# Kernel optimization log

Measured on AMD Instinct MI355X. Metric: run time of the kernel, lower is better.

## Reference

```python
import jax, jax.numpy as jnp
import numpy as np

NODE_DIM = 256
OUTPUT_DIM = 256
NUM_HOPS = 4
NUM_NODES = 25000
NUM_EDGES = 400000
NUM_TYPES = 10
FEAT_DIM = 32


def setup_inputs() -> dict:
    key = jax.random.key(0)
    ks = jax.random.split(key, 12)
    nodes = jax.random.normal(ks[0], (NUM_NODES, FEAT_DIM), dtype=jnp.float32)
    edges = jax.random.randint(ks[1], (2, NUM_EDGES), 0, NUM_NODES, dtype=jnp.int64)
    node_types = jax.random.randint(ks[2], (NUM_NODES,), 0, NUM_TYPES, dtype=jnp.int64)
    s = 0.02
    type_emb = jax.random.normal(ks[3], (NUM_TYPES, NODE_DIM), dtype=jnp.float32) * s
    W_proj = jax.random.normal(ks[4], (FEAT_DIM, NODE_DIM), dtype=jnp.float32) * s
    b_proj = jnp.zeros((NODE_DIM,), dtype=jnp.float32)
    W_msg = jax.random.normal(ks[5], (NUM_HOPS, 2 * NODE_DIM, NODE_DIM), dtype=jnp.float32) * s
    b_msg = jnp.zeros((NUM_HOPS, NODE_DIM), dtype=jnp.float32)
    W_upd = jax.random.normal(ks[6], (NUM_HOPS, 2 * NODE_DIM, NODE_DIM), dtype=jnp.float32) * s
    b_upd = jnp.zeros((NUM_HOPS, NODE_DIM), dtype=jnp.float32)
    W_out = jax.random.normal(ks[7], (NODE_DIM, OUTPUT_DIM), dtype=jnp.float32) * s
    b_out = jnp.zeros((OUTPUT_DIM,), dtype=jnp.float32)
    return {"nodes": nodes, "edges": edges, "node_types": node_types,
            "type_emb": type_emb, "W_proj": W_proj, "b_proj": b_proj,
            "W_msg": W_msg, "b_msg": b_msg, "W_upd": W_upd, "b_upd": b_upd,
            "W_out": W_out, "b_out": b_out}


def reference(nodes, edges, node_types, type_emb, W_proj, b_proj,
              W_msg, b_msg, W_upd, b_upd, W_out, b_out):
    n = nodes.shape[0]
    src, dst = edges[0], edges[1]
    # initial node states: linear proj + type embedding
    h = nodes @ W_proj + b_proj + type_emb[node_types]  # [N, D]
    for i in range(NUM_HOPS):
        edge_feat = jnp.concatenate([h[src], h[dst]], axis=1)      # [E, 2D]
        messages = edge_feat @ W_msg[i] + b_msg[i]                 # [E, D]
        agg = jax.ops.segment_sum(messages, dst, num_segments=n)   # [N, D]
        h = jax.nn.relu(jnp.concatenate([h, agg], axis=1) @ W_upd[i] + b_upd[i])
    graph_embedding = jnp.max(h, axis=0)                           # [D]
    return graph_embedding @ W_out + b_out                          # [output_dim]
```

## Files before the change

### kernel.cpp

```cpp
#include <hip/hip_runtime.h>
#include <hip/hip_bf16.h>

#define NDIM 256
#define FDIM 32
#define HOPS 4
#define NPB 8

typedef __attribute__((ext_vector_type(8))) short short8;
typedef __attribute__((ext_vector_type(4))) float f32x4;
typedef __attribute__((ext_vector_type(2))) float f32x2;

__device__ inline float b2f(unsigned short u) {
    union { unsigned int i; float f; } v; v.i = ((unsigned int)u) << 16; return v.f;
}
__device__ inline unsigned short f2b(float f) {
    union { float f; unsigned int i; } v; v.f = f;
    unsigned int r = v.i + 0x7FFF + ((v.i >> 16) & 1);
    return (unsigned short)(r >> 16);
}
__device__ inline unsigned char f2fp8(float v) {
    return (unsigned char)(__builtin_amdgcn_cvt_pk_fp8_f32(v, v, 0, false) & 0xFF);
}

__global__ __launch_bounds__(256) void prep_mega_kernel(
        const int* __restrict__ dst, int* __restrict__ deg, int E, int histB,
        const float* __restrict__ Wm, const float* __restrict__ Wu,
        const float* __restrict__ bm,
        unsigned short* __restrict__ WtB,
        unsigned short* __restrict__ Am, unsigned short* __restrict__ BmT,
        float* __restrict__ cvec, int* __restrict__ geInt,
        unsigned char* __restrict__ h8row,
        const float* __restrict__ nodes, const int* __restrict__ node_types,
        const float* __restrict__ type_emb, const float* __restrict__ W_proj,
        const float* __restrict__ b_proj,
        unsigned short* __restrict__ h, unsigned char* __restrict__ h8, int n) {
    __shared__ float T[32][33];
    __shared__ float sb[256];
    int b = blockIdx.x;
    int t = threadIdx.x;

    if (b < histB) {
        int e = (b * 256 + t) * 4;
        if (e + 3 < E) {
            int4 d = *(const int4*)(dst + e);
            atomicAdd(&deg[d.x], 1);
            atomicAdd(&deg[d.y], 1);
            atomicAdd(&deg[d.z], 1);
            atomicAdd(&deg[d.w], 1);
        } else {
            for (int k = e; k < E; ++k) atomicAdd(&deg[dst[k]], 1);
        }
    } else if (b < histB + 773) {
        int bb = b - histB;
        if (bb < 256) {
            int hop = bb >> 6;
            int rem = bb & 63;
            int k0 = (rem & 7) * 32, n0 = (rem >> 3) * 32;
            const float* src = Wu + (size_t)hop * 512 * 256;
            unsigned short* dstp = WtB + (size_t)hop * 256 * 256;
            int tr = t >> 5, tc = t & 31;
#pragma unroll
            for (int r = 0; r < 4; ++r) {
                int k = tr + r * 8;
                T[tc][k] = src[(size_t)(k0 + k) * 256 + n0 + tc];
            }
            __syncthreads();
#pragma unroll
            for (int r = 0; r < 4; ++r) {
                int nn = tr + r * 8;
                dstp[(size_t)(n0 + nn) * 256 + k0 + tc] = f2b(T[nn][tc]);
            }
        } else if (bb < 260) {
            int hop = bb - 256;
            sb[t] = bm[hop * 256 + t];
            __syncthreads();
            const float* B = Wu + (size_t)hop * 512 * 256 + (size_t)256 * 256;
            float acc = 0.f;
#pragma unroll 8
            for (int j = 0; j < 256; ++j) acc += sb[j] * B[(size_t)j * 256 + t];
            cvec[hop * 256 + t] = acc;
        } else if (bb == 260) {
            geInt[t] = 0;
            h8row[t] = 0;
        } else if (bb < 517) {
            size_t base = (size_t)(bb - 261) * 2048 + (size_t)t * 8;
            float4 a0 = *(const float4*)(Wm + base);
            float4 a1 = *(const float4*)(Wm + base + 4);
            ushort4 o0, o1;
            o0.x = f2b(a0.x); o0.y = f2b(a0.y); o0.z = f2b(a0.z); o0.w = f2b(a0.w);
            o1.x = f2b(a1.x); o1.y = f2b(a1.y); o1.z = f2b(a1.z); o1.w = f2b(a1.w);
            *(ushort4*)(Am + base) = o0;
            *(ushort4*)(Am + base + 4) = o1;
        } else {
            int tb = bb - 517;
            int hop = tb >> 6;
            int rem = tb & 63;
            int j0 = (rem & 7) * 32, n0 = (rem >> 3) * 32;
            const float* srcp = Wu + (size_t)hop * 512 * 256 + (size_t)256 * 256;
            unsigned short* dstp = BmT + (size_t)hop * 256 * 256;
            int tr = t >> 5, tc = t & 31;
#pragma unroll
            for (int r = 0; r < 4; ++r) {
                int j = tr + r * 8;
                T[tc][j] = srcp[(size_t)(j0 + j) * 256 + n0 + tc];
            }
            __syncthreads();
#pragma unroll
            for (int r = 0; r < 4; ++r) {
                int nn = tr + r * 8;
                dstp[(size_t)(n0 + nn) * 256 + j0 + tc] = f2b(T[nn][tc]);
            }
        }
    } else {
        int v0 = (b - histB - 773) * NPB;
        {
            int j = t >> 5, f = t & 31;
            int v = v0 + j;
            sb[t] = (v < n) ? nodes[(size_t)v * FDIM + f] : 0.f;
        }
        __syncthreads();
        float acc[NPB];
#pragma unroll
        for (int j = 0; j < NPB; ++j) {
            int v = v0 + j;
            acc[j] = (v < n) ? (b_proj[t] + type_emb[(size_t)node_types[v] * NDIM + t]) : 0.f;
        }
#pragma unroll 4
        for (int k = 0; k < FDIM; ++k) {
            float wv = W_proj[(size_t)k * NDIM + t];
#pragma unroll
            for (int j = 0; j < NPB; ++j)
                acc[j] += sb[j * FDIM + k] * wv;
        }
#pragma unroll
        for (int j = 0; j < NPB; ++j) {
            int v = v0 + j;
            if (v < n) {
                h[(size_t)v * NDIM + t] = f2b(acc[j]);
                h8[(size_t)v * NDIM + t] = f2fp8(acc[j]);
            }
        }
    }
}

__global__ __launch_bounds__(1024) void scan1_mm_kernel(
        const int* __restrict__ deg, int* __restrict__ rowptr,
        int* __restrict__ bsum, int nch, int n,
        const unsigned short* __restrict__ Am, const unsigned short* __restrict__ BmT,
        unsigned short* __restrict__ WtA, unsigned short* __restrict__ WtC) {
    int t = threadIdx.x;
    int b = blockIdx.x;
    if (b < nch) {
        __shared__ int wsum[16];
        int i = b * 1024 + t;
        int v = 0;
        if (i < n) v = (deg[i] + 7) & ~7;
        int lane = t & 63, wid = t >> 6;
        int x = v;
#pragma unroll
        for (int d = 1; d < 64; d <<= 1) {
            int u = __shfl_up(x, d, 64);
            if (lane >= d) x += u;
        }
        if (lane == 63) wsum[wid] = x;
        __syncthreads();
        if (wid == 0) {
            int ws = (lane < 16) ? wsum[lane] : 0;
#pragma unroll
            for (int d = 1; d < 16; d <<= 1) {
                int u = __shfl_up(ws, d, 64);
                if (lane >= d) ws += u;
            }
            if (lane < 16) wsum[lane] = ws;
        }
        __syncthreads();
        int excl = (wid > 0 ? wsum[wid - 1] : 0) + x - v;
        if (i < n) rowptr[i] = excl;
        if (t == 1023) bsum[b] = wsum[15];
        return;
    }

    int m = b - nch;
    int hop = m >> 1, which = m & 1;
    const unsigned short* A = Am + (size_t)m * 65536;
    const unsigned short* B = BmT + (size_t)hop * 65536;
    unsigned short* W = (which ? WtC : WtA) + (size_t)hop * 65536;
    int wave = t >> 6, lane = t & 63;
    int l16 = lane & 15, quad = lane >> 4;
    int k0 = (wave & 3) * 64;
    int n0 = (wave >> 2) * 64;
    f32x4 acc[4][4];
#pragma unroll
    for (int i = 0; i < 4; ++i)
#pragma unroll
        for (int j = 0; j < 4; ++j) acc[i][j] = (f32x4)(0.f);

    for (int j0 = 0; j0 < 256; j0 += 32) {
        short8 af[4], bfr[4];
#pragma unroll
        for (int kt = 0; kt < 4; ++kt)
            af[kt] = *(const short8*)(A + (size_t)(k0 + kt * 16 + l16) * 256 + j0 + quad * 8);
#pragma unroll
        for (int nt = 0; nt < 4; ++nt)
            bfr[nt] = *(const short8*)(B + (size_t)(n0 + nt * 16 + l16) * 256 + j0 + quad * 8);
#pragma unroll
        for (int kt = 0; kt < 4; ++kt)
#pragma unroll
            for (int nt = 0; nt < 4; ++nt)
                acc[kt][nt] = __builtin_amdgcn_mfma_f32_16x16x32_bf16(af[kt], bfr[nt], acc[kt][nt], 0, 0, 0);
    }
#pragma unroll
    for (int kt = 0; kt < 4; ++kt)
#pragma unroll
        for (int nt = 0; nt < 4; ++nt) {
            int k = k0 + kt * 16 + quad * 4;
            int nn = n0 + nt * 16 + l16;
            ushort4 o;
            o.x = f2b(acc[kt][nt][0]); o.y = f2b(acc[kt][nt][1]);
            o.z = f2b(acc[kt][nt][2]); o.w = f2b(acc[kt][nt][3]);
            *(ushort4*)&W[(size_t)nn * 256 + k] = o;
        }
}

__global__ __launch_bounds__(1024) void scan2_kernel(
        int* __restrict__ rowptr, int* __restrict__ cursor,
        const int* __restrict__ bsum, int nch, int n) {
    __shared__ int soff, stot;
    int t = threadIdx.x;
    int b = blockIdx.x;
    if (t < 64) {
        int s = (t < nch) ? bsum[t] : 0;
        int x = s;
#pragma unroll
        for (int d = 1; d < 64; d <<= 1) {
            int u = __shfl_up(x, d, 64);
            if (t >= d) x += u;
        }
        if (t == 63) stot = x;
        if (t == b) soff = x - s;
    }
    __syncthreads();
    int i = b * 1024 + t;
    if (i < n) {
        int r = rowptr[i] + soff;
        rowptr[i] = r;
        cursor[i] = r;
    }
    if (b == 0 && t == 0) rowptr[n] = stot;
}

__global__ void fillpad_kernel(const int* __restrict__ src, const int* __restrict__ dst,
                               int* __restrict__ cursor,
                               const int* __restrict__ rowptr, const int* __restrict__ deg,
                               int* __restrict__ col, int E, int fillB, int n) {
    int b = blockIdx.x;
    int t = threadIdx.x;
    if (b < fillB) {
        int e = b * 256 + t;
        if (e < E) {
            int d = dst[e];
            int p = atomicAdd(&cursor[d], 1);
            col[p] = src[e];
        }
    } else {
        int v = (b - fillB) * 256 + t;
        if (v < n) {
            int s = rowptr[v] + deg[v];
            int e0 = rowptr[v + 1];
            for (int i = s; i < e0; ++i) col[i] = n;
        }
    }
}

__global__ __launch_bounds__(256) void agg_kernel(const unsigned char* __restrict__ h8,
                                                  const int* __restrict__ rowptr,
                                                  const int* __restrict__ col,
                                                  unsigned short* __restrict__ S, int n) {
    int wave = threadIdx.x >> 6;
    int lane = threadIdx.x & 63;
    int half = lane >> 5;
    int hl = lane & 31;
    int v = blockIdx.x * 8 + wave * 2 + half;
    if (v >= n) return;
    int beg = rowptr[v], end = rowptr[v + 1];
    float a[8];
#pragma unroll
    for (int e = 0; e < 8; ++e) a[e] = 0.f;
    int cofs = hl * 8;
    int i = beg;
    for (; i + 16 <= end; i += 16) {
        int4 c4[4];
        c4[0] = *(const int4*)(col + i);
        c4[1] = *(const int4*)(col + i + 4);
        c4[2] = *(const int4*)(col + i + 8);
        c4[3] = *(const int4*)(col + i + 12);
        const int* cc = (const int*)c4;
        uint2 x[16];
#pragma unroll
        for (int j = 0; j < 16; ++j)
            x[j] = *(const uint2*)(h8 + (size_t)cc[j] * NDIM + cofs);
#pragma unroll
        for (int j = 0; j < 16; ++j) {
            f32x2 p0 = __builtin_amdgcn_cvt_pk_f32_fp8(x[j].x, false);
            f32x2 p1 = __builtin_amdgcn_cvt_pk_f32_fp8(x[j].x, true);
            f32x2 p2 = __builtin_amdgcn_cvt_pk_f32_fp8(x[j].y, false);
            f32x2 p3 = __builtin_amdgcn_cvt_pk_f32_fp8(x[j].y, true);
            a[0] += p0[0]; a[1] += p0[1]; a[2] += p1[0]; a[3] += p1[1];
            a[4] += p2[0]; a[5] += p2[1]; a[6] += p3[0]; a[7] += p3[1];
        }
    }
    for (; i < end; i += 8) {
        int4 c4[2];
        c4[0] = *(const int4*)(col + i);
        c4[1] = *(const int4*)(col + i + 4);
        const int* cc = (const int*)c4;
        uint2 x[8];
#pragma unroll
        for (int j = 0; j < 8; ++j)
            x[j] = *(const uint2*)(h8 + (size_t)cc[j] * NDIM + cofs);
#pragma unroll
        for (int j = 0; j < 8; ++j) {
            f32x2 p0 = __builtin_amdgcn_cvt_pk_f32_fp8(x[j].x, false);
            f32x2 p1 = __builtin_amdgcn_cvt_pk_f32_fp8(x[j].x, true);
            f32x2 p2 = __builtin_amdgcn_cvt_pk_f32_fp8(x[j].y, false);
            f32x2 p3 = __builtin_amdgcn_cvt_pk_f32_fp8(x[j].y, true);
            a[0] += p0[0]; a[1] += p0[1]; a[2] += p1[0]; a[3] += p1[1];
            a[4] += p2[0]; a[5] += p2[1]; a[6] += p3[0]; a[7] += p3[1];
        }
    }
    uint4 o;
    unsigned short* op = (unsigned short*)&o;
#pragma unroll
    for (int e = 0; e < 8; ++e) op[e] = f2b(a[e]);
    *(uint4*)&S[(size_t)v * NDIM + cofs] = o;
}

#define BM 128
#define BN 64
#define BK 64

template <bool LAST>
__global__ __launch_bounds__(256, 4) void gemm_hop_kernel(const unsigned short* __restrict__ S,
                                                          const unsigned short* __restrict__ hcur,
                                                          const int* __restrict__ deg,
                                                          const unsigned short* __restrict__ WtA,
                                                          const unsigned short* __restrict__ WtB,
                                                          const unsigned short* __restrict__ WtC,
                                                          const float* __restrict__ bupd,
                                                          const float* __restrict__ cvec,
                                                          unsigned short* __restrict__ Out,
                                                          unsigned char* __restrict__ Out8,
                                                          int* __restrict__ geInt, int n) {
    __shared__ unsigned short As[BM * BK];
    __shared__ unsigned short Bs[BN * BK];
    __shared__ unsigned short Cs[BN * BK];
    __shared__ int smax[BN];
    int t = threadIdx.x;
    int lane = t & 63;
    int w = t >> 6;
    int wm = w >> 1, wn = w & 1;
    int quad = lane >> 4, l16 = lane & 15;
    int row0 = blockIdx.x * BM;
    int n0 = blockIdx.y * BN;

    if (LAST) {
        if (t < BN) smax[t] = 0;
    }

    f32x4 acc1[4][2], acc2[4][2];
#pragma unroll
    for (int i = 0; i < 4; ++i)
#pragma unroll
        for (int j = 0; j < 2; ++j) { acc1[i][j] = (f32x4)(0.f); acc2[i][j] = (f32x4)(0.f); }

    for (int k0 = 0; k0 < NDIM; k0 += BK) {
        __syncthreads();
#pragma unroll
        for (int h2 = 0; h2 < 4; ++h2) {
            int c = t + h2 * 256;
            int r = c >> 3;
            int cb = (c & 7) ^ (r & 7);
            int grow = row0 + r; if (grow >= n) grow = n - 1;
            __builtin_amdgcn_global_load_lds(
                (const unsigned int*)(S + (size_t)grow * NDIM + k0 + cb * 8),
                (unsigned int*)(As + (size_t)(h2 * 256 + w * 64) * 8), 16, 0, 0);
        }
#pragma unroll
        for (int h2 = 0; h2 < 2; ++h2) {
            int c = t + h2 * 256;
            int r = c >> 3;
            int cb = (c & 7) ^ (r & 7);
            __builtin_amdgcn_global_load_lds(
                (const unsigned int*)(WtA + (size_t)(n0 + r) * NDIM + k0 + cb * 8),
                (unsigned int*)(Bs + (size_t)(h2 * 256 + w * 64) * 8), 16, 0, 0);
        }
        __syncthreads();
#pragma unroll
        for (int ks = 0; ks < BK; ks += 32) {
            short8 af[4], bf[2];
#pragma unroll
            for (int mt = 0; mt < 4; ++mt) {
                int ar = wm * 64 + mt * 16 + l16;
                int acb = ((ks >> 3) + quad) ^ (ar & 7);
                af[mt] = *(const short8*)&As[ar * BK + acb * 8];
            }
#pragma unroll
            for (int nt = 0; nt < 2; ++nt) {
                int br = wn * 32 + nt * 16 + l16;
                int bcb = ((ks >> 3) + quad) ^ (br & 7);
                bf[nt] = *(const short8*)&Bs[br * BK + bcb * 8];
            }
#pragma unroll
            for (int mt = 0; mt < 4; ++mt)
#pragma unroll
                for (int nt = 0; nt < 2; ++nt)
                    acc1[mt][nt] = __builtin_amdgcn_mfma_f32_16x16x32_bf16(af[mt], bf[nt], acc1[mt][nt], 0, 0, 0);
        }
    }
    for (int k0 = 0; k0 < NDIM; k0 += BK) {
        __syncthreads();
#pragma unroll
        for (int h2 = 0; h2 < 4; ++h2) {
            int c = t + h2 * 256;
            int r = c >> 3;
            int cb = (c & 7) ^ (r & 7);
            int grow = row0 + r; if (grow >= n) grow = n - 1;
            __builtin_amdgcn_global_load_lds(
                (const unsigned int*)(hcur + (size_t)grow * NDIM + k0 + cb * 8),
                (unsigned int*)(As + (size_t)(h2 * 256 + w * 64) * 8), 16, 0, 0);
        }
#pragma unroll
        for (int h2 = 0; h2 < 2; ++h2) {
            int c = t + h2 * 256;
            int r = c >> 3;
            int cb = (c & 7) ^ (r & 7);
            size_t widx = (size_t)(n0 + r) * NDIM + k0 + cb * 8;
            __builtin_amdgcn_global_load_lds(
                (const unsigned int*)(WtB + widx),
                (unsigned int*)(Bs + (size_t)(h2 * 256 + w * 64) * 8), 16, 0, 0);
            __builtin_amdgcn_global_load_lds(
                (const unsigned int*)(WtC + widx),
                (unsigned int*)(Cs + (size_t)(h2 * 256 + w * 64) * 8), 16, 0, 0);
        }
        __syncthreads();
#pragma unroll
        for (int ks = 0; ks < BK; ks += 32) {
            short8 af[4], bf[2], cf[2];
#pragma unroll
            for (int mt = 0; mt < 4; ++mt) {
                int ar = wm * 64 + mt * 16 + l16;
                int acb = ((ks >> 3) + quad) ^ (ar & 7);
                af[mt] = *(const short8*)&As[ar * BK + acb * 8];
            }
#pragma unroll
            for (int nt = 0; nt < 2; ++nt) {
                int br = wn * 32 + nt * 16 + l16;
                int bcb = ((ks >> 3) + quad) ^ (br & 7);
                bf[nt] = *(const short8*)&Bs[br * BK + bcb * 8];
                cf[nt] = *(const short8*)&Cs[br * BK + bcb * 8];
            }
#pragma unroll
            for (int mt = 0; mt < 4; ++mt)
#pragma unroll
                for (int nt = 0; nt < 2; ++nt) {
                    acc1[mt][nt] = __builtin_amdgcn_mfma_f32_16x16x32_bf16(af[mt], bf[nt], acc1[mt][nt], 0, 0, 0);
                    acc2[mt][nt] = __builtin_amdgcn_mfma_f32_16x16x32_bf16(af[mt], cf[nt], acc2[mt][nt], 0, 0, 0);
                }
        }
    }
#pragma unroll
    for (int mt = 0; mt < 4; ++mt) {
#pragma unroll
        for (int nt = 0; nt < 2; ++nt) {
            int lcol = wn * 32 + nt * 16 + l16;
            int col = n0 + lcol;
            float bu = bupd[col];
            float cv = cvec[col];
            float cmax = 0.f;
#pragma unroll
            for (int r = 0; r < 4; ++r) {
                int row = row0 + wm * 64 + mt * 16 + quad * 4 + r;
                if (row < n) {
                    float dg = (float)deg[row];
                    float v = fmaxf(acc1[mt][nt][r] + dg * (acc2[mt][nt][r] + cv) + bu, 0.f);
                    Out[(size_t)row * NDIM + col] = f2b(v);
                    if (!LAST) Out8[(size_t)row * NDIM + col] = f2fp8(v);
                    if (LAST) cmax = fmaxf(cmax, v);
                }
            }
            if (LAST) atomicMax(&smax[lcol], __float_as_int(cmax));
        }
    }
    if (LAST) {
        __syncthreads();
        if (t < BN) atomicMax(&geInt[n0 + t], smax[t]);
    }
}

__global__ __launch_bounds__(1024) void out_kernel(const float* __restrict__ ge,
                                                   const float* __restrict__ W_out,
                                                   const float* __restrict__ b_out,
                                                   float* __restrict__ out) {
    __shared__ float red[4][NDIM];
    int t = threadIdx.x & 255;
    int g = threadIdx.x >> 8;
    float acc = 0.f;
#pragma unroll 8
    for (int kk = 0; kk < 64; ++kk) {
        int k = g * 64 + kk;
        acc += ge[k] * W_out[k * NDIM + t];
    }
    red[g][t] = acc;
    __syncthreads();
    if (g == 0)
        out[t] = b_out[t] + red[0][t] + red[1][t] + red[2][t] + red[3][t];
}

extern "C" void kernel_launch(void* const* d_in, const int* in_sizes, int n_in,
                              void* d_out, int out_size, void* d_ws, size_t ws_size,
                              hipStream_t stream) {
    const float* nodes      = (const float*)d_in[0];
    const int*   edges      = (const int*)d_in[1];
    const int*   node_types = (const int*)d_in[2];
    const float* type_emb   = (const float*)d_in[3];
    const float* W_proj     = (const float*)d_in[4];
    const float* b_proj     = (const float*)d_in[5];
    const float* W_msg      = (const float*)d_in[6];
    const float* b_msg      = (const float*)d_in[7];
    const float* W_upd      = (const float*)d_in[8];
    const float* b_upd      = (const float*)d_in[9];
    const float* W_out      = (const float*)d_in[10];
    const float* b_out      = (const float*)d_in[11];

    int n = in_sizes[2];
    int E = in_sizes[1] / 2;
    const int* src = edges;
    const int* dst = edges + E;

    size_t off = 0;
    auto alloc = [&](size_t bytes) {
        void* p = (char*)d_ws + off;
        off += (bytes + 255) & ~(size_t)255;
        return p;
    };
    int* deg    = (int*)alloc((size_t)(n + 4096) * 4);
    int* rowptr = (int*)alloc((size_t)(n + 1) * 4);
    int* cursor = (int*)alloc((size_t)n * 4);
    int* bsum   = (int*)alloc((size_t)256 * 4);
    int* col    = (int*)alloc((size_t)(E + 8 * n) * 4);
    unsigned short* WtA = (unsigned short*)alloc((size_t)HOPS * 256 * 256 * 2);
    unsigned short* WtB = (unsigned short*)alloc((size_t)HOPS * 256 * 256 * 2);
    unsigned short* WtC = (unsigned short*)alloc((size_t)HOPS * 256 * 256 * 2);
    unsigned short* Am  = (unsigned short*)alloc((size_t)8 * 256 * 256 * 2);
    unsigned short* BmT = (unsigned short*)alloc((size_t)HOPS * 256 * 256 * 2);
    float* cvec = (float*)alloc((size_t)HOPS * 256 * 4);
    int* geInt  = (int*)alloc((size_t)256 * 4);
    unsigned short* hA  = (unsigned short*)alloc((size_t)(n + 1) * NDIM * 2);
    unsigned short* hB  = (unsigned short*)alloc((size_t)(n + 1) * NDIM * 2);
    unsigned short* Sb  = (unsigned short*)alloc((size_t)n * NDIM * 2);
    unsigned char* h8   = (unsigned char*)alloc((size_t)(n + 1) * NDIM);

    hipMemsetAsync(deg, 0, (size_t)(n + 4096) * 4, stream);
    int hb = (E + 1023) / 1024;
    int eb = (E + 255) / 256;
    int pb = (n + 255) / 256;
    int ib = (n + NPB - 1) / NPB;
    int nch = (n + 1023) / 1024;
    prep_mega_kernel<<<hb + 773 + ib, 256, 0, stream>>>(
        dst, deg, E, hb,
        W_msg, W_upd, b_msg, WtB, Am, BmT, cvec, geInt, h8 + (size_t)n * NDIM,
        nodes, node_types, type_emb, W_proj, b_proj, hA, h8, n);
    scan1_mm_kernel<<<nch + 8, 1024, 0, stream>>>(deg, rowptr, bsum, nch, n, Am, BmT, WtA, WtC);
    scan2_kernel<<<nch, 1024, 0, stream>>>(rowptr, cursor, bsum, nch, n);
    fillpad_kernel<<<eb + pb, 256, 0, stream>>>(src, dst, cursor, rowptr, deg, col, E, eb, n);

    unsigned short* h  = hA;
    unsigned short* ho = hB;
    int gx = (n + BM - 1) / BM;
    dim3 ggrid(gx, NDIM / BN);
    for (int i = 0; i < HOPS; ++i) {
        agg_kernel<<<(n + 7) / 8, 256, 0, stream>>>(h8, rowptr, col, Sb, n);
        size_t wofs = (size_t)i * 256 * 256;
        if (i == HOPS - 1)
            gemm_hop_kernel<true><<<ggrid, 256, 0, stream>>>(
                Sb, h, deg, WtA + wofs, WtB + wofs, WtC + wofs,
                b_upd + (size_t)i * NDIM, cvec + (size_t)i * NDIM, ho, h8, geInt, n);
        else
            gemm_hop_kernel<false><<<ggrid, 256, 0, stream>>>(
                Sb, h, deg, WtA + wofs, WtB + wofs, WtC + wofs,
                b_upd + (size_t)i * NDIM, cvec + (size_t)i * NDIM, ho, h8, geInt, n);
        unsigned short* tmp = h; h = ho; ho = tmp;
    }
    out_kernel<<<1, 1024, 0, stream>>>((const float*)geInt, W_out, b_out, (float*)d_out);
}
```

Before: 332.2 us.

## Remap GEMM blocks per XCD, prefetch agg column indices, double projection nodes per block

The hop GEMM moves to a 1D grid whose block index is remapped so that the four column tiles of a row tile land on the same XCD, improving L2 reuse of the A/S rows. The aggregation kernel software-prefetches the next 16 column indices while gathering the current batch, hiding index-load latency. The initial projection processes 16 nodes per block instead of 8, amortizing weight loads. The remap relies on the round-robin block-to-XCD dispatch and leaves some blocks idle at the padded tail.

```diff
diff --git a/kernel.cpp b/kernel.cpp
--- a/kernel.cpp
+++ b/kernel.cpp
@@ -4,7 +4,7 @@
 #define NDIM 256
 #define FDIM 32
 #define HOPS 4
-#define NPB 8
+#define NPB 16
 
 typedef __attribute__((ext_vector_type(8))) short short8;
 typedef __attribute__((ext_vector_type(4))) float f32x4;
@@ -35,7 +35,7 @@
         const float* __restrict__ b_proj,
         unsigned short* __restrict__ h, unsigned char* __restrict__ h8, int n) {
     __shared__ float T[32][33];
-    __shared__ float sb[256];
+    __shared__ float sb[512];
     int b = blockIdx.x;
     int t = threadIdx.x;
 
@@ -113,10 +113,12 @@
         }
     } else {
         int v0 = (b - histB - 773) * NPB;
-        {
-            int j = t >> 5, f = t & 31;
+#pragma unroll
+        for (int s = 0; s < 2; ++s) {
+            int idx = t + s * 256;
+            int j = idx >> 5, f = idx & 31;
             int v = v0 + j;
-            sb[t] = (v < n) ? nodes[(size_t)v * FDIM + f] : 0.f;
+            sb[idx] = (v < n) ? nodes[(size_t)v * FDIM + f] : 0.f;
         }
         __syncthreads();
         float acc[NPB];
@@ -288,25 +290,50 @@
     for (int e = 0; e < 8; ++e) a[e] = 0.f;
     int cofs = hl * 8;
     int i = beg;
-    for (; i + 16 <= end; i += 16) {
-        int4 c4[4];
-        c4[0] = *(const int4*)(col + i);
-        c4[1] = *(const int4*)(col + i + 4);
-        c4[2] = *(const int4*)(col + i + 8);
-        c4[3] = *(const int4*)(col + i + 12);
-        const int* cc = (const int*)c4;
-        uint2 x[16];
-#pragma unroll
-        for (int j = 0; j < 16; ++j)
-            x[j] = *(const uint2*)(h8 + (size_t)cc[j] * NDIM + cofs);
-#pragma unroll
-        for (int j = 0; j < 16; ++j) {
-            f32x2 p0 = __builtin_amdgcn_cvt_pk_f32_fp8(x[j].x, false);
-            f32x2 p1 = __builtin_amdgcn_cvt_pk_f32_fp8(x[j].x, true);
-            f32x2 p2 = __builtin_amdgcn_cvt_pk_f32_fp8(x[j].y, false);
-            f32x2 p3 = __builtin_amdgcn_cvt_pk_f32_fp8(x[j].y, true);
-            a[0] += p0[0]; a[1] += p0[1]; a[2] += p1[0]; a[3] += p1[1];
-            a[4] += p2[0]; a[5] += p2[1]; a[6] += p3[0]; a[7] += p3[1];
+    if (i + 16 <= end) {
+        int4 cA0 = *(const int4*)(col + i);
+        int4 cA1 = *(const int4*)(col + i + 4);
+        int4 cA2 = *(const int4*)(col + i + 8);
+        int4 cA3 = *(const int4*)(col + i + 12);
+        for (; i + 32 <= end; i += 16) {
+            int4 cB0 = *(const int4*)(col + i + 16);
+            int4 cB1 = *(const int4*)(col + i + 20);
+            int4 cB2 = *(const int4*)(col + i + 24);
+            int4 cB3 = *(const int4*)(col + i + 28);
+            int4 c4[4] = {cA0, cA1, cA2, cA3};
+            const int* cc = (const int*)c4;
+            uint2 x[16];
+#pragma unroll
+            for (int j = 0; j < 16; ++j)
+                x[j] = *(const uint2*)(h8 + (size_t)cc[j] * NDIM + cofs);
+#pragma unroll
+            for (int j = 0; j < 16; ++j) {
+                f32x2 p0 = __builtin_amdgcn_cvt_pk_f32_fp8(x[j].x, false);
+                f32x2 p1 = __builtin_amdgcn_cvt_pk_f32_fp8(x[j].x, true);
+                f32x2 p2 = __builtin_amdgcn_cvt_pk_f32_fp8(x[j].y, false);
+                f32x2 p3 = __builtin_amdgcn_cvt_pk_f32_fp8(x[j].y, true);
+                a[0] += p0[0]; a[1] += p0[1]; a[2] += p1[0]; a[3] += p1[1];
+                a[4] += p2[0]; a[5] += p2[1]; a[6] += p3[0]; a[7] += p3[1];
+            }
+            cA0 = cB0; cA1 = cB1; cA2 = cB2; cA3 = cB3;
+        }
+        {
+            int4 c4[4] = {cA0, cA1, cA2, cA3};
+            const int* cc = (const int*)c4;
+            uint2 x[16];
+#pragma unroll
+            for (int j = 0; j < 16; ++j)
+                x[j] = *(const uint2*)(h8 + (size_t)cc[j] * NDIM + cofs);
+#pragma unroll
+            for (int j = 0; j < 16; ++j) {
+                f32x2 p0 = __builtin_amdgcn_cvt_pk_f32_fp8(x[j].x, false);
+                f32x2 p1 = __builtin_amdgcn_cvt_pk_f32_fp8(x[j].x, true);
+                f32x2 p2 = __builtin_amdgcn_cvt_pk_f32_fp8(x[j].y, false);
+                f32x2 p3 = __builtin_amdgcn_cvt_pk_f32_fp8(x[j].y, true);
+                a[0] += p0[0]; a[1] += p0[1]; a[2] += p1[0]; a[3] += p1[1];
+                a[4] += p2[0]; a[5] += p2[1]; a[6] += p3[0]; a[7] += p3[1];
+            }
+            i += 16;
         }
     }
     for (; i < end; i += 8) {
@@ -355,13 +382,22 @@
     __shared__ unsigned short Bs[BN * BK];
     __shared__ unsigned short Cs[BN * BK];
     __shared__ int smax[BN];
+
+    int gx = (n + BM - 1) / BM;
+    int bid = blockIdx.x;
+    int xcd = bid & 7;
+    int q = bid >> 3;
+    int g = (q >> 2) * 8 + xcd;
+    int by = q & 3;
+    if (g >= gx) return;
+    int row0 = g * BM;
+    int n0 = by * BN;
+
     int t = threadIdx.x;
     int lane = t & 63;
     int w = t >> 6;
     int wm = w >> 1, wn = w & 1;
     int quad = lane >> 4, l16 = lane & 15;
-    int row0 = blockIdx.x * BM;
-    int n0 = blockIdx.y * BN;
 
     if (LAST) {
         if (t < BN) smax[t] = 0;
@@ -577,7 +613,7 @@
     unsigned short* h  = hA;
     unsigned short* ho = hB;
     int gx = (n + BM - 1) / BM;
-    dim3 ggrid(gx, NDIM / BN);
+    int ggrid = 8 * ((gx + 7) / 8) * 4;
     for (int i = 0; i < HOPS; ++i) {
         agg_kernel<<<(n + 7) / 8, 256, 0, stream>>>(h8, rowptr, col, Sb, n);
         size_t wofs = (size_t)i * 256 * 256;
```

Measured after the change: 328.5 us. About the same (-1.1%).
